# Kernel optimization log

Measured on AMD Instinct MI355X. Metric: run time of the kernel, lower is better.

The kernel has to match this reference:

```python
import jax, jax.numpy as jnp
import numpy as np

KH, KW = 3, 3          # kernel_size
SH, SW = 1, 1          # stride
PH, PW = 1, 1          # padding
NCODEBOOKS = 16
SUBVEC = 36            # (64*3*3)/16
K = 16                 # codewords per codebook (4 tree levels)


def _unfold(x):
    """torch.nn.functional.unfold equivalent: (b,c,h,w) -> (b, c*KH*KW, oh, ow),
    feature dim ordered channel-major (c, ki, kj) like torch."""
    b, c, h, w = x.shape
    xp = jnp.pad(x, ((0, 0), (0, 0), (PH, PH), (PW, PW)))
    oh = (h + 2 * PH - KH) // SH + 1
    ow = (w + 2 * PW - KW) // SW + 1
    patches = [xp[:, :, i:i + (oh - 1) * SH + 1:SH, j:j + (ow - 1) * SW + 1:SW]
               for i in range(KH) for j in range(KW)]
    cols = jnp.stack(patches, axis=2)              # (b, c, KH*KW, oh, ow)
    return cols.reshape(b, c * KH * KW, oh, ow)


def setup_inputs() -> dict:
    key = jax.random.key(0)
    k1, k2, k3, k4, k5 = jax.random.split(key, 5)
    return {
        "x": jax.random.normal(k1, (16, 64, 56, 56), dtype=jnp.float32),
        "split_idxs": jax.random.randint(k2, (NCODEBOOKS, 4), 0, SUBVEC, dtype=jnp.int32),
        "split_vals": jax.random.normal(k3, (NCODEBOOKS, 4, K // 2), dtype=jnp.float32),
        "lookup_tables": jax.random.normal(k4, (NCODEBOOKS, K, 64), dtype=jnp.float32),
        "bias": jax.random.normal(k5, (64,), dtype=jnp.float32),
    }


def reference(x, split_idxs, split_vals, lookup_tables, bias):
    b = x.shape[0]
    cols = _unfold(x)                              # (b, d, oh, ow)
    _, d, oh, ow = cols.shape
    # torch: cols.permute(0,2,1).flatten(0,1) with L=oh*ow row-major
    xf = cols.reshape(b, d, oh * ow).transpose(0, 2, 1).reshape(-1, d)  # (n, d)
    n = xf.shape[0]
    xs = xf.reshape(n, NCODEBOOKS, SUBVEC)
    car = jnp.arange(NCODEBOOKS)
    # Hierarchical 4-level threshold encoding (vectorized over all codebooks):
    # at level t, a point in bucket e compares feature split_idxs[c,t] against
    # split_vals[c,t,e]; new bucket = 2*e + (v >= thr)  (matches the serial
    # bucket-list construction: '<' -> left child, '>=' -> right child).
    enc = jnp.zeros((n, NCODEBOOKS), dtype=jnp.int32)
    for t in range(4):
        v = xs[:, car, split_idxs[:, t]]           # (n, NCODEBOOKS)
        thr = split_vals[car[None, :], t, enc]     # (n, NCODEBOOKS)
        enc = 2 * enc + (v >= thr).astype(jnp.int32)
    # LUT gather-sum (equivalent to one_hot(enc) @ lookup_tables[i], summed)
    gathered = lookup_tables[car[None, :], enc]    # (n, NCODEBOOKS, out_ch)
    out = gathered.sum(axis=1) + bias              # (n, out_ch)
    out = out.reshape(b, oh, ow, -1).transpose(0, 3, 1, 2)
    return out
```

## Files before the change

### kernel.cpp

```cpp
#include <hip/hip_runtime.h>

static constexpr int W56     = 56;
static constexpr int SPATIAL = 56 * 56;
static constexpr int CH      = 64;
static constexpr int NCB     = 16;

__global__ __launch_bounds__(256) void maddness_conv(
    const float* __restrict__ x,
    const int*   __restrict__ split_idxs,
    const float* __restrict__ split_vals,
    const float* __restrict__ lut,
    const float* __restrict__ bias,
    float*       __restrict__ out)
{
    __shared__ float4 lutq[NCB * 16 * 5];
    __shared__ float  svals[512];
    __shared__ int    selChOff[64];
    __shared__ int    selDy[64];
    __shared__ int    selDx[64];
    __shared__ float4 biasq4[4];

    const int tid  = threadIdx.x;
    const int q    = blockIdx.x & 3;
    const int pblk = blockIdx.x >> 2;

    const float4* lut4 = reinterpret_cast<const float4*>(lut);
    #pragma unroll
    for (int i = 0; i < 4; ++i) {
        int idx = tid + i * 256;
        int row = idx >> 2;
        int j   = idx & 3;
        lutq[row * 5 + j] = lut4[(row << 4) + (q << 2) + j];
    }
    svals[tid]       = split_vals[tid];
    svals[tid + 256] = split_vals[tid + 256];
    if (tid < 64) {
        int g  = (tid >> 2) * 36 + split_idxs[tid];
        int ch = g / 9;
        int k  = g - ch * 9;
        int ki = k / 3;
        int dy = ki - 1;
        int dx = (k - ki * 3) - 1;
        selChOff[tid] = ch * SPATIAL;
        selDy[tid]    = dy;
        selDx[tid]    = dx;
    }
    if (tid < 4) biasq4[tid] = reinterpret_cast<const float4*>(bias)[(q << 2) + tid];
    __syncthreads();

    const int p  = pblk * 256 + tid;
    const int b  = p / SPATIAL;
    const int s  = p - b * SPATIAL;
    const int y  = s / W56;
    const int xc = s - y * W56;
    const float* __restrict__ xb = x + b * (CH * SPATIAL);

    float v[NCB][4];
    #pragma unroll
    for (int cb = 0; cb < NCB; ++cb) {
        #pragma unroll
        for (int t = 0; t < 4; ++t) {
            const int i  = cb * 4 + t;
            const int yy = y  + selDy[i];
            const int xx = xc + selDx[i];
            const bool ok = ((unsigned)yy < (unsigned)W56) & ((unsigned)xx < (unsigned)W56);
            const int yyc = min(max(yy, 0), W56 - 1);
            const int xxc = min(max(xx, 0), W56 - 1);
            const float lv = xb[selChOff[i] + yyc * W56 + xxc];
            v[cb][t] = ok ? lv : 0.0f;
        }
    }

    float4 a0 = biasq4[0], a1 = biasq4[1], a2 = biasq4[2], a3 = biasq4[3];

    #pragma unroll
    for (int cb = 0; cb < NCB; ++cb) {
        int e = 0;
        #pragma unroll
        for (int t = 0; t < 4; ++t) {
            e = (e << 1) | (v[cb][t] >= svals[(cb * 4 + t) * 8 + e] ? 1 : 0);
        }
        const float4* row = &lutq[(cb * 16 + e) * 5];
        a0 += row[0];
        a1 += row[1];
        a2 += row[2];
        a3 += row[3];
    }

    float* __restrict__ op = out + b * (CH * SPATIAL) + (q * 16) * SPATIAL + s;
    op[ 0 * SPATIAL] = a0.x; op[ 1 * SPATIAL] = a0.y; op[ 2 * SPATIAL] = a0.z; op[ 3 * SPATIAL] = a0.w;
    op[ 4 * SPATIAL] = a1.x; op[ 5 * SPATIAL] = a1.y; op[ 6 * SPATIAL] = a1.z; op[ 7 * SPATIAL] = a1.w;
    op[ 8 * SPATIAL] = a2.x; op[ 9 * SPATIAL] = a2.y; op[10 * SPATIAL] = a2.z; op[11 * SPATIAL] = a2.w;
    op[12 * SPATIAL] = a3.x; op[13 * SPATIAL] = a3.y; op[14 * SPATIAL] = a3.z; op[15 * SPATIAL] = a3.w;
}

extern "C" void kernel_launch(void* const* d_in, const int* in_sizes, int n_in,
                              void* d_out, int out_size, void* d_ws, size_t ws_size,
                              hipStream_t stream) {
    const float* x  = (const float*)d_in[0];
    const int*   si = (const int*)  d_in[1];
    const float* sv = (const float*)d_in[2];
    const float* lt = (const float*)d_in[3];
    const float* bs = (const float*)d_in[4];
    float* o = (float*)d_out;

    maddness_conv<<<dim3(196 * 4), dim3(256), 0, stream>>>(x, si, sv, lt, bs, o);
}
```

Measured before the change: 80.44 us.

## Split encoding across wavefronts, share codes via LDS, accumulate LUT in half precision

Each block now handles 64 pixels. Every wavefront encodes 4 of the 16 codebooks, so each pixel's gathers run once instead of four times, one per output quarter. The packed codes are exchanged through shared memory, and each wavefront then accumulates 16 output channels from a lookup table stored in LDS as fp16. Split thresholds are kept in scalar registers and the tree is walked with selects instead of dependent LDS lookups. The trade-off is that fp16 LUT values and fp16 accumulation lose precision, and the whole LUT is loaded into every block.

```diff
diff --git a/kernel.cpp b/kernel.cpp
--- a/kernel.cpp
+++ b/kernel.cpp
@@ -1,97 +1,129 @@
 #include <hip/hip_runtime.h>
+#include <hip/hip_fp16.h>
 
-static constexpr int W56     = 56;
-static constexpr int SPATIAL = 56 * 56;
-static constexpr int CH      = 64;
-static constexpr int NCB     = 16;
+static constexpr int W56 = 56;
+static constexpr int SP  = 56 * 56;
+static constexpr int CHN = 64;
 
-__global__ __launch_bounds__(256) void maddness_conv(
+__device__ __forceinline__ float rfl_f(float v) {
+    return __int_as_float(__builtin_amdgcn_readfirstlane(__float_as_int(v)));
+}
+
+__global__ __launch_bounds__(256, 3) void maddness_conv(
     const float* __restrict__ x,
-    const int*   __restrict__ split_idxs,
-    const float* __restrict__ split_vals,
+    const int*   __restrict__ si,
+    const float* __restrict__ sv,
     const float* __restrict__ lut,
     const float* __restrict__ bias,
     float*       __restrict__ out)
 {
-    __shared__ float4 lutq[NCB * 16 * 5];
-    __shared__ float  svals[512];
-    __shared__ int    selChOff[64];
-    __shared__ int    selDy[64];
-    __shared__ int    selDx[64];
-    __shared__ float4 biasq4[4];
+    __shared__ __half2        lutLds[256 * 36];
+    __shared__ unsigned short codes[256];
 
     const int tid  = threadIdx.x;
-    const int q    = blockIdx.x & 3;
-    const int pblk = blockIdx.x >> 2;
+    const int part = tid >> 6;
+    const int lane = tid & 63;
+
+    const int b  = blockIdx.x / 49;
+    const int s  = (blockIdx.x - b * 49) * 64 + lane;
+    const int y  = s / W56;
+    const int xc = s - y * W56;
+    const float* __restrict__ xb = x + b * (CHN * SP);
+
+    float v[4][4];
+    #pragma unroll
+    for (int c = 0; c < 4; ++c) {
+        #pragma unroll
+        for (int t = 0; t < 4; ++t) {
+            const int cb = part * 4 + c;
+            const int i  = cb * 4 + t;
+            const int g  = __builtin_amdgcn_readfirstlane(si[i]) + cb * 36;
+            const int ch = g / 9;
+            const int k9 = g - ch * 9;
+            const int ki = k9 / 3;
+            const int dy = ki - 1;
+            const int dx = (k9 - ki * 3) - 1;
+            const int yy = y + dy, xx = xc + dx;
+            const bool ok = ((unsigned)yy < (unsigned)W56) & ((unsigned)xx < (unsigned)W56);
+            const int yyc = min(max(yy, 0), W56 - 1);
+            const int xxc = min(max(xx, 0), W56 - 1);
+            const float lv = xb[ch * SP + yyc * W56 + xxc];
+            v[c][t] = ok ? lv : 0.0f;
+        }
+    }
+
+    float T0[4], T1[4][2], T2[4][4], T3[4][8];
+    #pragma unroll
+    for (int c = 0; c < 4; ++c) {
+        const int base = (part * 4 + c) * 32;
+        T0[c] = rfl_f(sv[base]);
+        #pragma unroll
+        for (int j = 0; j < 2; ++j) T1[c][j] = rfl_f(sv[base + 8  + j]);
+        #pragma unroll
+        for (int j = 0; j < 4; ++j) T2[c][j] = rfl_f(sv[base + 16 + j]);
+        #pragma unroll
+        for (int j = 0; j < 8; ++j) T3[c][j] = rfl_f(sv[base + 24 + j]);
+    }
 
     const float4* lut4 = reinterpret_cast<const float4*>(lut);
     #pragma unroll
-    for (int i = 0; i < 4; ++i) {
-        int idx = tid + i * 256;
-        int row = idx >> 2;
-        int j   = idx & 3;
-        lutq[row * 5 + j] = lut4[(row << 4) + (q << 2) + j];
+    for (int i = 0; i < 16; ++i) {
+        const int idx = tid + i * 256;
+        const int row = idx >> 4, k = idx & 15;
+        const float4 f = lut4[idx];
+        lutLds[row * 36 + 2 * k]     = __float22half2_rn(make_float2(f.x, f.y));
+        lutLds[row * 36 + 2 * k + 1] = __float22half2_rn(make_float2(f.z, f.w));
     }
-    svals[tid]       = split_vals[tid];
-    svals[tid + 256] = split_vals[tid + 256];
-    if (tid < 64) {
-        int g  = (tid >> 2) * 36 + split_idxs[tid];
-        int ch = g / 9;
-        int k  = g - ch * 9;
-        int ki = k / 3;
-        int dy = ki - 1;
-        int dx = (k - ki * 3) - 1;
-        selChOff[tid] = ch * SPATIAL;
-        selDy[tid]    = dy;
-        selDx[tid]    = dx;
+
+    unsigned code = 0;
+    #pragma unroll
+    for (int c = 0; c < 4; ++c) {
+        const bool b0 = v[c][0] >= T0[c];
+        const float t1 = b0 ? T1[c][1] : T1[c][0];
+        const bool b1 = v[c][1] >= t1;
+        const float s01 = b1 ? T2[c][1] : T2[c][0];
+        const float s23 = b1 ? T2[c][3] : T2[c][2];
+        const bool b2 = v[c][2] >= (b0 ? s23 : s01);
+        const float w0 = b2 ? T3[c][1] : T3[c][0];
+        const float w1 = b2 ? T3[c][3] : T3[c][2];
+        const float w2 = b2 ? T3[c][5] : T3[c][4];
+        const float w3 = b2 ? T3[c][7] : T3[c][6];
+        const float z0 = b1 ? w1 : w0;
+        const float z1 = b1 ? w3 : w2;
+        const bool b3 = v[c][3] >= (b0 ? z1 : z0);
+        const int e = ((int)b0 << 3) | ((int)b1 << 2) | ((int)b2 << 1) | (int)b3;
+        code |= (unsigned)e << (4 * c);
     }
-    if (tid < 4) biasq4[tid] = reinterpret_cast<const float4*>(bias)[(q << 2) + tid];
+    codes[part * 64 + lane] = (unsigned short)code;
     __syncthreads();
 
-    const int p  = pblk * 256 + tid;
-    const int b  = p / SPATIAL;
-    const int s  = p - b * SPATIAL;
-    const int y  = s / W56;
-    const int xc = s - y * W56;
-    const float* __restrict__ xb = x + b * (CH * SPATIAL);
+    const int q = part;
+    const unsigned cd0 = codes[lane];
+    const unsigned cd1 = codes[64 + lane];
+    const unsigned cd2 = codes[128 + lane];
+    const unsigned cd3 = codes[192 + lane];
 
-    float v[NCB][4];
+    __half2 acc[8];
     #pragma unroll
-    for (int cb = 0; cb < NCB; ++cb) {
+    for (int r = 0; r < 8; ++r) acc[r] = __half2{__half(0.0f), __half(0.0f)};
+
+    #pragma unroll
+    for (int cb = 0; cb < 16; ++cb) {
+        const unsigned cw = (cb < 4) ? cd0 : (cb < 8) ? cd1 : (cb < 12) ? cd2 : cd3;
+        const int e = (int)((cw >> ((cb & 3) * 4)) & 15u);
+        const __half2* __restrict__ row = &lutLds[(cb * 16 + e) * 36 + q * 8];
         #pragma unroll
-        for (int t = 0; t < 4; ++t) {
-            const int i  = cb * 4 + t;
-            const int yy = y  + selDy[i];
-            const int xx = xc + selDx[i];
-            const bool ok = ((unsigned)yy < (unsigned)W56) & ((unsigned)xx < (unsigned)W56);
-            const int yyc = min(max(yy, 0), W56 - 1);
-            const int xxc = min(max(xx, 0), W56 - 1);
-            const float lv = xb[selChOff[i] + yyc * W56 + xxc];
-            v[cb][t] = ok ? lv : 0.0f;
-        }
+        for (int r = 0; r < 8; ++r) acc[r] += row[r];
     }
 
-    float4 a0 = biasq4[0], a1 = biasq4[1], a2 = biasq4[2], a3 = biasq4[3];
-
+    float* __restrict__ op = out + b * (CHN * SP) + (q * 16) * SP + s;
+    const float* __restrict__ bq = bias + q * 16;
     #pragma unroll
-    for (int cb = 0; cb < NCB; ++cb) {
-        int e = 0;
-        #pragma unroll
-        for (int t = 0; t < 4; ++t) {
-            e = (e << 1) | (v[cb][t] >= svals[(cb * 4 + t) * 8 + e] ? 1 : 0);
-        }
-        const float4* row = &lutq[(cb * 16 + e) * 5];
-        a0 += row[0];
-        a1 += row[1];
-        a2 += row[2];
-        a3 += row[3];
+    for (int r = 0; r < 8; ++r) {
+        const float2 f = __half22float2(acc[r]);
+        op[(2 * r)     * SP] = f.x + bq[2 * r];
+        op[(2 * r + 1) * SP] = f.y + bq[2 * r + 1];
     }
-
-    float* __restrict__ op = out + b * (CH * SPATIAL) + (q * 16) * SPATIAL + s;
-    op[ 0 * SPATIAL] = a0.x; op[ 1 * SPATIAL] = a0.y; op[ 2 * SPATIAL] = a0.z; op[ 3 * SPATIAL] = a0.w;
-    op[ 4 * SPATIAL] = a1.x; op[ 5 * SPATIAL] = a1.y; op[ 6 * SPATIAL] = a1.z; op[ 7 * SPATIAL] = a1.w;
-    op[ 8 * SPATIAL] = a2.x; op[ 9 * SPATIAL] = a2.y; op[10 * SPATIAL] = a2.z; op[11 * SPATIAL] = a2.w;
-    op[12 * SPATIAL] = a3.x; op[13 * SPATIAL] = a3.y; op[14 * SPATIAL] = a3.z; op[15 * SPATIAL] = a3.w;
 }
 
 extern "C" void kernel_launch(void* const* d_in, const int* in_sizes, int n_in,
@@ -104,5 +136,5 @@
     const float* bs = (const float*)d_in[4];
     float* o = (float*)d_out;
 
-    maddness_conv<<<dim3(196 * 4), dim3(256), 0, stream>>>(x, si, sv, lt, bs, o);
+    maddness_conv<<<dim3(784), dim3(256), 0, stream>>>(x, si, sv, lt, bs, o);
 }
```

Result: faster. 77.47 us (-3.7%).
